# Optimization experiments

Hardware: AMD Instinct MI355X
Metric: run time of the kernel (lower is better)

The kernel has to match this reference:

```python
import jax, jax.numpy as jnp
import numpy as np

D_MODEL = 1024
NUM_HEAD = 16
D_K = D_MODEL // NUM_HEAD
B, S = 2, 2048


def setup_inputs() -> dict:
    key = jax.random.key(0)
    ks = jax.random.split(key, 12)
    s = 1.0 / np.sqrt(D_MODEL)
    return {
        "x_q": jax.random.normal(ks[0], (B, S, D_MODEL), jnp.float32),
        "x_k": jax.random.normal(ks[1], (B, S, D_MODEL), jnp.float32),
        "x_v": jax.random.normal(ks[2], (B, S, D_MODEL), jnp.float32),
        "mask": jax.random.randint(ks[3], (B, S, S), 0, 2, jnp.int32),
        "Wq": jax.random.uniform(ks[4], (D_MODEL, D_MODEL), jnp.float32, -s, s),
        "bq": jax.random.uniform(ks[5], (D_MODEL,), jnp.float32, -s, s),
        "Wk": jax.random.uniform(ks[6], (D_MODEL, D_MODEL), jnp.float32, -s, s),
        "bk": jax.random.uniform(ks[7], (D_MODEL,), jnp.float32, -s, s),
        "Wv": jax.random.uniform(ks[8], (D_MODEL, D_MODEL), jnp.float32, -s, s),
        "bv": jax.random.uniform(ks[9], (D_MODEL,), jnp.float32, -s, s),
        "Wo": jax.random.uniform(ks[10], (D_MODEL, D_MODEL), jnp.float32, -s, s),
        "bo": jax.random.uniform(ks[11], (D_MODEL,), jnp.float32, -s, s),
    }


def reference(x_q, x_k, x_v, mask, Wq, bq, Wk, bk, Wv, bv, Wo, bo):
    # projections -> [B, H, S, d_k]
    def proj(x, W, b):
        y = x @ W.T + b
        return y.reshape(B, -1, NUM_HEAD, D_K).transpose(0, 2, 1, 3)

    q = proj(x_q, Wq, bq)
    k = proj(x_k, Wk, bk)
    v = proj(x_v, Wv, bv)
    scale = 1.0 / np.sqrt(D_K).astype(np.float32)
    scores = jnp.einsum("bhqd,bhkd->bhqk", q, k) * scale
    scores = jnp.where(mask[:, None, :, :] == 0, jnp.float32(-1e9), scores)
    p = jax.nn.softmax(scores, axis=-1)  # dropout is identity in eval mode
    attn = jnp.einsum("bhqk,bhkd->bhqd", p, v)
    concat = attn.transpose(0, 2, 1, 3).reshape(B, S, D_MODEL)
    return concat @ Wo.T + bo
```

## Files before the change

### kernel.cpp

```cpp
#include <hip/hip_runtime.h>
#include <cstdint>
#include <cstddef>

#define D_MODELX 1024
#define NUM_HEADX 16
#define D_KX 64
#define BBX 2
#define SSX 2048
#define M_TOK 4096
#define MBYTE (1u << 20)

typedef __attribute__((ext_vector_type(8))) short short8;
typedef __attribute__((ext_vector_type(4))) short short4v;
typedef __attribute__((ext_vector_type(4))) float float4v;

__device__ __forceinline__ short f2bf(float f) {
  unsigned u = __builtin_bit_cast(unsigned, f);
  u = u + 0x7FFFu + ((u >> 16) & 1u);
  return (short)(u >> 16);
}

__global__ void mask_bits_kernel(const int* __restrict__ mask, unsigned* __restrict__ mbits) {
  int i = blockIdx.x * blockDim.x + threadIdx.x;
  bool v = mask[i] != 0;
  unsigned long long bal = __ballot(v);
  int lane = threadIdx.x & 63;
  if (lane == 0)       mbits[i >> 5] = (unsigned)bal;
  else if (lane == 32) mbits[i >> 5] = (unsigned)(bal >> 32);
}

__global__ void cvt_w4_kernel(const float* __restrict__ w0, const float* __restrict__ w1,
                              const float* __restrict__ w2, const float* __restrict__ w3,
                              short* __restrict__ o0, short* __restrict__ o1,
                              short* __restrict__ o2, short* __restrict__ o3) {
  int z = blockIdx.y;
  const float* in = (z == 0) ? w0 : (z == 1) ? w1 : (z == 2) ? w2 : w3;
  short* out = (z == 0) ? o0 : (z == 1) ? o1 : (z == 2) ? o2 : o3;
  int i = blockIdx.x * blockDim.x + threadIdx.x;
  float4v v = ((const float4v*)in)[i];
  short4v s;
  s[0] = f2bf(v[0]); s[1] = f2bf(v[1]); s[2] = f2bf(v[2]); s[3] = f2bf(v[3]);
  ((short4v*)out)[i] = s;
}

__global__ void cvt_x3_kernel(const float* __restrict__ x0, const float* __restrict__ x1,
                              const float* __restrict__ x2,
                              short* __restrict__ o0, short* __restrict__ o1,
                              short* __restrict__ o2) {
  int z = blockIdx.y;
  const float* in = (z == 0) ? x0 : (z == 1) ? x1 : x2;
  short* out = (z == 0) ? o0 : (z == 1) ? o1 : o2;
  int i = blockIdx.x * blockDim.x + threadIdx.x;
  float4v v = ((const float4v*)in)[i];
  short4v s;
  s[0] = f2bf(v[0]); s[1] = f2bf(v[1]); s[2] = f2bf(v[2]); s[3] = f2bf(v[3]);
  ((short4v*)out)[i] = s;
}

#define GBK 64
#define GLDT (GBK + 8)

__device__ __forceinline__ void gemm_body(const short* __restrict__ A,
                                          const short* __restrict__ Bw,
                                          const float* __restrict__ bias,
                                          float oscale, void* __restrict__ outp, int mode) {
  __shared__ short lds_a[128][GLDT];
  __shared__ short lds_b[128][GLDT];
  const int tid = threadIdx.x;
  const int lane = tid & 63;
  const int wid = tid >> 6;
  const int wm = wid >> 1, wn = wid & 1;
  const int bn = blockIdx.x, bm = blockIdx.y;
  const int l15 = lane & 15, lg = lane >> 4;

  float4v acc[4][4];
#pragma unroll
  for (int m = 0; m < 4; ++m)
#pragma unroll
    for (int n = 0; n < 4; ++n) acc[m][n] = (float4v){0.f, 0.f, 0.f, 0.f};

  for (int kt = 0; kt < 1024; kt += GBK) {
#pragma unroll
    for (int it = 0; it < 4; ++it) {
      int idx = it * 2048 + tid * 8;
      int row = idx >> 6, col = idx & 63;
      *(short8*)&lds_a[row][col] = *(const short8*)(A + (size_t)(bm * 128 + row) * 1024 + kt + col);
      *(short8*)&lds_b[row][col] = *(const short8*)(Bw + (size_t)(bn * 128 + row) * 1024 + kt + col);
    }
    __syncthreads();

    short8 af[4][2], bf[4][2];
#pragma unroll
    for (int m = 0; m < 4; ++m) {
      af[m][0] = *(const short8*)&lds_a[wm * 64 + m * 16 + l15][lg * 8];
      af[m][1] = *(const short8*)&lds_a[wm * 64 + m * 16 + l15][32 + lg * 8];
    }
#pragma unroll
    for (int n = 0; n < 4; ++n) {
      bf[n][0] = *(const short8*)&lds_b[wn * 64 + n * 16 + l15][lg * 8];
      bf[n][1] = *(const short8*)&lds_b[wn * 64 + n * 16 + l15][32 + lg * 8];
    }
#pragma unroll
    for (int m = 0; m < 4; ++m)
#pragma unroll
      for (int n = 0; n < 4; ++n) {
        acc[m][n] = __builtin_amdgcn_mfma_f32_16x16x32_bf16(af[m][0], bf[n][0], acc[m][n], 0, 0, 0);
        acc[m][n] = __builtin_amdgcn_mfma_f32_16x16x32_bf16(af[m][1], bf[n][1], acc[m][n], 0, 0, 0);
      }
    __syncthreads();
  }

#pragma unroll
  for (int n = 0; n < 4; ++n) {
    int col = bn * 128 + wn * 64 + n * 16 + l15;
    float bv = bias[col];
#pragma unroll
    for (int m = 0; m < 4; ++m) {
      if (mode == 2) {
        int base_row = bm * 128 + wm * 64 + m * 16 + lg * 4;
        int bidx = base_row >> 11, s = base_row & 2047;
        int h = col >> 6, d = col & 63;
        short4v sv;
#pragma unroll
        for (int r = 0; r < 4; ++r) sv[r] = f2bf(acc[m][n][r] + bv);
        *(short4v*)&((short*)outp)[(((size_t)(bidx * NUM_HEADX + h)) * D_KX + d) * SSX + s] = sv;
      } else {
#pragma unroll
        for (int r = 0; r < 4; ++r) {
          int row = bm * 128 + wm * 64 + m * 16 + lg * 4 + r;
          float val = (acc[m][n][r] + bv) * oscale;
          if (mode == 0) {
            int bidx = row >> 11, s = row & 2047;
            int h = col >> 6, d = col & 63;
            ((short*)outp)[(((size_t)(bidx * NUM_HEADX + h)) * SSX + s) * D_KX + d] = f2bf(val);
          } else {
            ((float*)outp)[(size_t)row * D_MODELX + col] = val;
          }
        }
      }
    }
  }
}

__global__ __launch_bounds__(256) void gemm_qkv_kernel(
    const short* __restrict__ xq, const short* __restrict__ xk, const short* __restrict__ xv,
    const short* __restrict__ wq, const short* __restrict__ wk, const short* __restrict__ wv,
    const float* __restrict__ bq, const float* __restrict__ bk, const float* __restrict__ bv,
    short* __restrict__ qo, short* __restrict__ ko, short* __restrict__ vo, float qs) {
  int z = blockIdx.z;
  const short* A = (z == 0) ? xq : (z == 1) ? xk : xv;
  const short* W = (z == 0) ? wq : (z == 1) ? wk : wv;
  const float* bi = (z == 0) ? bq : (z == 1) ? bk : bv;
  void* out = (z == 0) ? (void*)qo : (z == 1) ? (void*)ko : (void*)vo;
  float os = (z == 0) ? qs : 1.0f;
  int mode = (z == 2) ? 2 : 0;
  gemm_body(A, W, bi, os, out, mode);
}

__global__ __launch_bounds__(256) void gemm_one_kernel(const short* __restrict__ A,
                                                       const short* __restrict__ W,
                                                       const float* __restrict__ bias,
                                                       float os, void* __restrict__ out, int mode) {
  gemm_body(A, W, bias, os, out, mode);
}

__device__ __forceinline__ int swzk(int row, int col) {
  int byte = (row << 7) + (col << 1);
  return (byte ^ ((row & 7) << 4)) >> 1;
}

__global__ __launch_bounds__(256) void attn_kernel(const short* __restrict__ q_ws,
                                                   const short* __restrict__ k_ws,
                                                   const short* __restrict__ vT_ws,
                                                   const unsigned* __restrict__ mbits,
                                                   short* __restrict__ attn_ws) {
  __shared__ short k_lds[2][64 * 64];
  __shared__ short vT_lds[2][64 * 64];
  __shared__ short p_lds[4][16 * 64];

  const int tid = threadIdx.x;
  const int lane = tid & 63;
  const int w = tid >> 6;
  const int l15 = lane & 15, lg = lane >> 4;
  const int bid0 = blockIdx.x;
  const int bid = ((bid0 & 7) << 7) | (bid0 >> 3);
  const int qt = bid & 31;
  const int bh = bid >> 5;
  const int b = bh >> 4;
  const int h = bh & 15;

  short* pw = p_lds[w];
  const int qrow = qt * 64 + w * 16;

  const int srow = tid >> 2;
  const int scol = (tid & 3) << 4;
  const short* Kb = k_ws + (size_t)bh * SSX * D_KX;
  const short* Vb = vT_ws + (size_t)bh * D_KX * SSX;

  short8 qf[2];
#pragma unroll
  for (int f = 0; f < 2; ++f)
    qf[f] = *(const short8*)(q_ws + ((size_t)bh * SSX + qrow + l15) * D_KX + f * 32 + lg * 8);

  float4v acc[4];
#pragma unroll
  for (int db = 0; db < 4; ++db) acc[db] = (float4v){0.f, 0.f, 0.f, 0.f};
  float m_run = -INFINITY, l_part = 0.f;

  short8 kr0, kr1, vr0, vr1;
  auto loadt = [&](int kb) {
    const short* kp = Kb + (size_t)(kb + srow) * D_KX + scol;
    kr0 = *(const short8*)kp;
    kr1 = *(const short8*)(kp + 8);
    const short* vp = Vb + (size_t)srow * SSX + kb + scol;
    vr0 = *(const short8*)vp;
    vr1 = *(const short8*)(vp + 8);
  };
  auto storet = [&](int bf) {
    *(short8*)&k_lds[bf][swzk(srow, scol)] = kr0;
    *(short8*)&k_lds[bf][swzk(srow, scol + 8)] = kr1;
    *(short8*)&vT_lds[bf][swzk(srow, scol)] = vr0;
    *(short8*)&vT_lds[bf][swzk(srow, scol + 8)] = vr1;
  };

  const unsigned* mrow = mbits + ((size_t)b * SSX + qrow + l15) * (SSX / 32);
  unsigned long long mw = *(const unsigned long long*)mrow, mwn;

  loadt(0);
  storet(0);
  loadt(64);
  __syncthreads();

  for (int t = 0; t < 32; ++t) {
    const int cur = t & 1;
    const short* kl = k_lds[cur];
    const short* vl = vT_lds[cur];

    float p[4][4];
#pragma unroll
    for (int kf = 0; kf < 4; ++kf) {
      short8 k0 = *(const short8*)&kl[swzk(kf * 16 + l15, lg * 8)];
      short8 k1 = *(const short8*)&kl[swzk(kf * 16 + l15, 32 + lg * 8)];
      float4v f = (float4v){0.f, 0.f, 0.f, 0.f};
      f = __builtin_amdgcn_mfma_f32_16x16x32_bf16(k0, qf[0], f, 0, 0, 0);
      f = __builtin_amdgcn_mfma_f32_16x16x32_bf16(k1, qf[1], f, 0, 0, 0);
#pragma unroll
      for (int r = 0; r < 4; ++r) p[kf][r] = f[r];
    }

    if (t < 31) storet(1 - cur);
    if (t < 30) loadt((t + 2) * 64);
    if (t < 31) mwn = *(const unsigned long long*)(mrow + 2 * (t + 1));

    float tmax = fmaxf(fmaxf(fmaxf(p[0][0], p[0][1]), fmaxf(p[0][2], p[0][3])),
                       fmaxf(fmaxf(p[1][0], p[1][1]), fmaxf(p[1][2], p[1][3])));
    tmax = fmaxf(tmax, fmaxf(fmaxf(fmaxf(p[2][0], p[2][1]), fmaxf(p[2][2], p[2][3])),
                             fmaxf(fmaxf(p[3][0], p[3][1]), fmaxf(p[3][2], p[3][3]))));
    if (!__all(tmax - m_run <= 8.0f)) {
      tmax = fmaxf(tmax, __shfl_xor(tmax, 16));
      tmax = fmaxf(tmax, __shfl_xor(tmax, 32));
      float mn = fmaxf(m_run, tmax);
      float corr = __builtin_amdgcn_exp2f(m_run - mn);
      m_run = mn;
      l_part *= corr;
#pragma unroll
      for (int db = 0; db < 4; ++db)
#pragma unroll
        for (int r = 0; r < 4; ++r) acc[db][r] *= corr;
    }

    unsigned long long sh = mw >> (lg * 4);
    unsigned mlo = (unsigned)sh, mhi = (unsigned)(sh >> 32);

#pragma unroll
    for (int kf = 0; kf < 4; ++kf) {
      float pv_[4];
#pragma unroll
      for (int r = 0; r < 4; ++r) {
        float pv = __builtin_amdgcn_exp2f(p[kf][r] - m_run);
        unsigned bit = (kf < 2 ? mlo : mhi) & (1u << ((kf & 1) * 16 + r));
        pv = bit ? pv : 0.0f;
        l_part += pv;
        pv_[r] = pv;
      }
      unsigned u0, u1;
      asm("v_cvt_pk_bf16_f32 %0, %1, %2" : "=v"(u0) : "v"(pv_[0]), "v"(pv_[1]));
      asm("v_cvt_pk_bf16_f32 %0, %1, %2" : "=v"(u1) : "v"(pv_[2]), "v"(pv_[3]));
      uint2 w2;
      w2.x = u0; w2.y = u1;
      *(uint2*)&pw[swzk(l15, kf * 16 + lg * 4)] = w2;
    }

#pragma unroll
    for (int db = 0; db < 4; ++db) {
#pragma unroll
      for (int c = 0; c < 2; ++c) {
        short8 vb = *(const short8*)&vl[swzk(db * 16 + l15, c * 32 + lg * 8)];
        short8 pa = *(const short8*)&pw[swzk(l15, c * 32 + lg * 8)];
        acc[db] = __builtin_amdgcn_mfma_f32_16x16x32_bf16(vb, pa, acc[db], 0, 0, 0);
      }
    }

    __syncthreads();
    mw = mwn;
  }

  l_part += __shfl_xor(l_part, 16);
  l_part += __shfl_xor(l_part, 32);
  float inv = 1.0f / l_part;

  size_t ttok = (size_t)b * SSX + qrow + l15;
#pragma unroll
  for (int db = 0; db < 4; ++db) {
    short4v sv;
#pragma unroll
    for (int r = 0; r < 4; ++r) sv[r] = f2bf(acc[db][r] * inv);
    *(short4v*)&attn_ws[ttok * D_MODELX + h * 64 + db * 16 + lg * 4] = sv;
  }
}

extern "C" void kernel_launch(void* const* d_in, const int* in_sizes, int n_in,
                              void* d_out, int out_size, void* d_ws, size_t ws_size,
                              hipStream_t stream) {
  const float* x_q = (const float*)d_in[0];
  const float* x_k = (const float*)d_in[1];
  const float* x_v = (const float*)d_in[2];
  const int*   mask = (const int*)d_in[3];
  const float* Wq = (const float*)d_in[4];
  const float* bq = (const float*)d_in[5];
  const float* Wk = (const float*)d_in[6];
  const float* bk = (const float*)d_in[7];
  const float* Wv = (const float*)d_in[8];
  const float* bv = (const float*)d_in[9];
  const float* Wo = (const float*)d_in[10];
  const float* bo = (const float*)d_in[11];

  const float QSCALE = 0.125f * 1.44269504089f;

  char* ws = (char*)d_ws;
  short* q_ws  = (short*)(ws + 0 * MBYTE);
  short* k_ws  = (short*)(ws + 8 * MBYTE);
  short* vT_ws = (short*)(ws + 16 * MBYTE);

  dim3 ggrid(D_MODELX / 128, M_TOK / 128);

  if (ws_size >= (size_t)56 * MBYTE) {
    short* wq_bf = (short*)(ws + 24 * MBYTE);
    short* wk_bf = (short*)(ws + 26 * MBYTE);
    short* wv_bf = (short*)(ws + 28 * MBYTE);
    short* wo_bf = (short*)(ws + 30 * MBYTE);
    short* xq_bf = (short*)(ws + 32 * MBYTE);
    short* xk_bf = (short*)(ws + 40 * MBYTE);
    short* xv_bf = (short*)(ws + 48 * MBYTE);
    short* attn_ws = (short*)(ws + 32 * MBYTE);
    unsigned* mbits = (unsigned*)(ws + 40 * MBYTE);

    cvt_w4_kernel<<<dim3(1024, 4), 256, 0, stream>>>(Wq, Wk, Wv, Wo, wq_bf, wk_bf, wv_bf, wo_bf);
    cvt_x3_kernel<<<dim3(4096, 3), 256, 0, stream>>>(x_q, x_k, x_v, xq_bf, xk_bf, xv_bf);

    dim3 qkvgrid(D_MODELX / 128, M_TOK / 128, 3);
    gemm_qkv_kernel<<<qkvgrid, 256, 0, stream>>>(xq_bf, xk_bf, xv_bf, wq_bf, wk_bf, wv_bf,
                                                 bq, bk, bv, q_ws, k_ws, vT_ws, QSCALE);

    mask_bits_kernel<<<(BBX * SSX * SSX) / 256, 256, 0, stream>>>(mask, mbits);

    attn_kernel<<<BBX * NUM_HEADX * (SSX / 64), 256, 0, stream>>>(q_ws, k_ws, vT_ws, mbits, attn_ws);

    gemm_one_kernel<<<ggrid, 256, 0, stream>>>(attn_ws, wo_bf, bo, 1.0f, d_out, 1);
  } else {
    unsigned* mbits = (unsigned*)(ws + 24 * MBYTE);
    short* w_bf = (short*)(ws + 25 * MBYTE);
    short* x_bf = (short*)(ws + 27 * MBYTE);
    short* attn_ws = (short*)(ws + 27 * MBYTE);

    mask_bits_kernel<<<(BBX * SSX * SSX) / 256, 256, 0, stream>>>(mask, mbits);

    cvt_w4_kernel<<<dim3(1024, 1), 256, 0, stream>>>(Wq, Wq, Wq, Wq, w_bf, w_bf, w_bf, w_bf);
    cvt_x3_kernel<<<dim3(4096, 1), 256, 0, stream>>>(x_q, x_q, x_q, x_bf, x_bf, x_bf);
    gemm_one_kernel<<<ggrid, 256, 0, stream>>>(x_bf, w_bf, bq, QSCALE, q_ws, 0);

    cvt_w4_kernel<<<dim3(1024, 1), 256, 0, stream>>>(Wk, Wk, Wk, Wk, w_bf, w_bf, w_bf, w_bf);
    cvt_x3_kernel<<<dim3(4096, 1), 256, 0, stream>>>(x_k, x_k, x_k, x_bf, x_bf, x_bf);
    gemm_one_kernel<<<ggrid, 256, 0, stream>>>(x_bf, w_bf, bk, 1.0f, k_ws, 0);

    cvt_w4_kernel<<<dim3(1024, 1), 256, 0, stream>>>(Wv, Wv, Wv, Wv, w_bf, w_bf, w_bf, w_bf);
    cvt_x3_kernel<<<dim3(4096, 1), 256, 0, stream>>>(x_v, x_v, x_v, x_bf, x_bf, x_bf);
    gemm_one_kernel<<<ggrid, 256, 0, stream>>>(x_bf, w_bf, bv, 1.0f, vT_ws, 2);

    attn_kernel<<<BBX * NUM_HEADX * (SSX / 64), 256, 0, stream>>>(q_ws, k_ws, vT_ws, mbits, attn_ws);

    cvt_w4_kernel<<<dim3(1024, 1), 256, 0, stream>>>(Wo, Wo, Wo, Wo, w_bf, w_bf, w_bf, w_bf);
    gemm_one_kernel<<<ggrid, 256, 0, stream>>>(attn_ws, w_bf, bo, 1.0f, d_out, 1);
  }
}
```

Baseline: 172.8 us.

## Load GEMM tiles directly into swizzled LDS and raise attention occupancy hint

The GEMM tile loads now use global_load_lds, which writes global data straight into LDS without a register round trip. The padded LDS layout is replaced by an XOR-swizzled layout so fragment reads avoid bank conflicts. B fragments are loaded per n inside the MFMA loop to cut register pressure. The attention kernel gains a launch-bounds minimum of four blocks per CU, which may force register spilling.

```diff
diff --git a/kernel.cpp b/kernel.cpp
--- a/kernel.cpp
+++ b/kernel.cpp
@@ -58,14 +58,17 @@
 }
 
 #define GBK 64
-#define GLDT (GBK + 8)
+
+__device__ __forceinline__ int swbg(int row, int colB) {
+  return row * 128 + (colB ^ ((row & 7) << 4));
+}
 
 __device__ __forceinline__ void gemm_body(const short* __restrict__ A,
                                           const short* __restrict__ Bw,
                                           const float* __restrict__ bias,
                                           float oscale, void* __restrict__ outp, int mode) {
-  __shared__ short lds_a[128][GLDT];
-  __shared__ short lds_b[128][GLDT];
+  __shared__ short lds_a[128 * 64];
+  __shared__ short lds_b[128 * 64];
   const int tid = threadIdx.x;
   const int lane = tid & 63;
   const int wid = tid >> 6;
@@ -73,6 +76,11 @@
   const int bn = blockIdx.x, bm = blockIdx.y;
   const int l15 = lane & 15, lg = lane >> 4;
 
+  const int s_row = tid >> 3;
+  const int s_cB = ((tid & 7) << 4) ^ ((s_row & 7) << 4);
+  const short* Abase = A + (size_t)(bm * 128) * 1024 + (s_cB >> 1);
+  const short* Bbase = Bw + (size_t)(bn * 128) * 1024 + (s_cB >> 1);
+
   float4v acc[4][4];
 #pragma unroll
   for (int m = 0; m < 4; ++m)
@@ -82,31 +90,34 @@
   for (int kt = 0; kt < 1024; kt += GBK) {
 #pragma unroll
     for (int it = 0; it < 4; ++it) {
-      int idx = it * 2048 + tid * 8;
-      int row = idx >> 6, col = idx & 63;
-      *(short8*)&lds_a[row][col] = *(const short8*)(A + (size_t)(bm * 128 + row) * 1024 + kt + col);
-      *(short8*)&lds_b[row][col] = *(const short8*)(Bw + (size_t)(bn * 128 + row) * 1024 + kt + col);
+      int row = it * 32 + s_row;
+      __builtin_amdgcn_global_load_lds(
+          (const uint32_t*)(Abase + (size_t)row * 1024 + kt),
+          (uint32_t*)(lds_a + (it * 256 + wid * 64) * 8), 16, 0, 0);
+      __builtin_amdgcn_global_load_lds(
+          (const uint32_t*)(Bbase + (size_t)row * 1024 + kt),
+          (uint32_t*)(lds_b + (it * 256 + wid * 64) * 8), 16, 0, 0);
     }
     __syncthreads();
 
-    short8 af[4][2], bf[4][2];
+    short8 af[4][2];
 #pragma unroll
     for (int m = 0; m < 4; ++m) {
-      af[m][0] = *(const short8*)&lds_a[wm * 64 + m * 16 + l15][lg * 8];
-      af[m][1] = *(const short8*)&lds_a[wm * 64 + m * 16 + l15][32 + lg * 8];
+      int row = wm * 64 + m * 16 + l15;
+      af[m][0] = *(const short8*)((const char*)lds_a + swbg(row, lg * 16));
+      af[m][1] = *(const short8*)((const char*)lds_a + swbg(row, 64 + lg * 16));
     }
 #pragma unroll
     for (int n = 0; n < 4; ++n) {
-      bf[n][0] = *(const short8*)&lds_b[wn * 64 + n * 16 + l15][lg * 8];
-      bf[n][1] = *(const short8*)&lds_b[wn * 64 + n * 16 + l15][32 + lg * 8];
-    }
-#pragma unroll
-    for (int m = 0; m < 4; ++m)
-#pragma unroll
-      for (int n = 0; n < 4; ++n) {
-        acc[m][n] = __builtin_amdgcn_mfma_f32_16x16x32_bf16(af[m][0], bf[n][0], acc[m][n], 0, 0, 0);
-        acc[m][n] = __builtin_amdgcn_mfma_f32_16x16x32_bf16(af[m][1], bf[n][1], acc[m][n], 0, 0, 0);
+      int rowb = wn * 64 + n * 16 + l15;
+      short8 b0 = *(const short8*)((const char*)lds_b + swbg(rowb, lg * 16));
+      short8 b1 = *(const short8*)((const char*)lds_b + swbg(rowb, 64 + lg * 16));
+#pragma unroll
+      for (int m = 0; m < 4; ++m) {
+        acc[m][n] = __builtin_amdgcn_mfma_f32_16x16x32_bf16(af[m][0], b0, acc[m][n], 0, 0, 0);
+        acc[m][n] = __builtin_amdgcn_mfma_f32_16x16x32_bf16(af[m][1], b1, acc[m][n], 0, 0, 0);
       }
+    }
     __syncthreads();
   }
 
@@ -169,11 +180,11 @@
   return (byte ^ ((row & 7) << 4)) >> 1;
 }
 
-__global__ __launch_bounds__(256) void attn_kernel(const short* __restrict__ q_ws,
-                                                   const short* __restrict__ k_ws,
-                                                   const short* __restrict__ vT_ws,
-                                                   const unsigned* __restrict__ mbits,
-                                                   short* __restrict__ attn_ws) {
+__global__ __launch_bounds__(256, 4) void attn_kernel(const short* __restrict__ q_ws,
+                                                      const short* __restrict__ k_ws,
+                                                      const short* __restrict__ vT_ws,
+                                                      const unsigned* __restrict__ mbits,
+                                                      short* __restrict__ attn_ws) {
   __shared__ short k_lds[2][64 * 64];
   __shared__ short vT_lds[2][64 * 64];
   __shared__ short p_lds[4][16 * 64];
```

Result: faster. 168.6 us (-2.4%).
